# Optimization experiments

Hardware: AMD Instinct MI355X
Metric: run time of the kernel (lower is better)

## Reference

```python
import jax, jax.numpy as jnp
import numpy as np

B, N, D, F, L, R = 16, 1024, 256, 128, 2, 2


def setup_inputs() -> dict:
    key = jax.random.key(0)
    ks = jax.random.split(key, 12)
    s = 0.05
    return {
        "node_embed": jax.random.normal(ks[0], (B, N, D), jnp.float32),
        "input_x": jax.random.normal(ks[1], (B, F), jnp.float32),
        "adj": jax.random.randint(ks[2], (R, B, N, N), 0, 2, jnp.int32),
        "WQi_w": jax.random.normal(ks[3], (L, F, F), jnp.float32) * s,
        "WQi_b": jnp.zeros((L, F), jnp.float32),
        "WQ_w": jax.random.normal(ks[4], (L, D + F, D), jnp.float32) * s,
        "WQ_b": jnp.zeros((L, D), jnp.float32),
        "WK_w": jax.random.normal(ks[5], (L, R, D + F, D), jnp.float32) * s,
        "WK_b": jnp.zeros((L, R, D), jnp.float32),
        "WV_w": jax.random.normal(ks[6], (L, R, D + F, D), jnp.float32) * s,
        "WV_b": jnp.zeros((L, R, D), jnp.float32),
        "WF_w": jax.random.normal(ks[7], (L, R * D, D), jnp.float32) * s,
        "WF_b": jnp.zeros((L, D), jnp.float32),
        "ln_g": jnp.ones((L, D), jnp.float32),
        "ln_b": jnp.zeros((L, D), jnp.float32),
    }


def _layer_norm(x, g, b, eps=1e-5):
    mu = jnp.mean(x, axis=-1, keepdims=True)
    var = jnp.var(x, axis=-1, keepdims=True)
    return (x - mu) * jax.lax.rsqrt(var + eps) * g + b


def reference(node_embed, input_x, adj, WQi_w, WQi_b, WQ_w, WQ_b,
              WK_w, WK_b, WV_w, WV_b, WF_w, WF_b, ln_g, ln_b):
    scale = 1.0 / (D ** 0.5)
    h = node_embed
    for l in range(L):
        # input feature projection, broadcast over nodes
        x1 = input_x @ WQi_w[l] + WQi_b[l]              # (B, F)
        x1 = jnp.broadcast_to(x1[:, None, :], (h.shape[0], h.shape[1], F))
        qc = jnp.concatenate([h, x1], axis=-1)          # (B, N, D+F)
        q = qc @ WQ_w[l] + WQ_b[l]                      # (B, N, D)
        outs = []
        for r in range(R):
            k = qc @ WK_w[l, r] + WK_b[l, r]            # (B, N, D)
            v = qc @ WV_w[l, r] + WV_b[l, r]            # (B, N, D)
            scores = jnp.einsum('bnd,bmd->bnm', q, k) * scale
            scores = jnp.where(adj[r] == 0, -1e9, scores)
            alpha = jax.nn.softmax(scores, axis=-1)
            outs.append(jnp.einsum('bnm,bmd->bnd', alpha, v))
        h_concat = jnp.concatenate(outs, axis=-1)       # (B, N, R*D)
        h_fused = jax.nn.relu(h_concat @ WF_w[l] + WF_b[l])
        h = _layer_norm(h + h_fused, ln_g[l], ln_b[l])
    return h
```

## Files before the change

kernel.cpp:

```cpp
#include <hip/hip_runtime.h>
#include <hip/hip_bf16.h>

#define BB 16
#define NN 1024
#define DD 256
#define FF_ 128
#define LL 2
#define RR 2
#define DF 384
#define MM (BB*NN)
#define NPROJ 1280
#define PK 768
#define CSC 0.09016844f

typedef __attribute__((ext_vector_type(8))) short s16x8;
typedef __attribute__((ext_vector_type(4))) float f32x4;
typedef __attribute__((ext_vector_type(16))) float f32x16;
typedef __attribute__((ext_vector_type(2))) unsigned int u32x2;
typedef __attribute__((ext_vector_type(4))) unsigned int u32x4;
typedef __attribute__((ext_vector_type(4))) unsigned short us16x4;

__device__ __forceinline__ unsigned short f2bf(float f){
  unsigned u = __builtin_bit_cast(unsigned, f);
  u += 0x7fff + ((u >> 16) & 1);
  return (unsigned short)(u >> 16);
}

__device__ __forceinline__ void gload16(const void* g, void* l){
  __builtin_amdgcn_global_load_lds(
      (const __attribute__((address_space(1))) unsigned int*)g,
      (__attribute__((address_space(3))) unsigned int*)l, 16, 0, 0);
}

#define MFMA16(a,b,c) __builtin_amdgcn_mfma_f32_16x16x32_bf16((a),(b),(c),0,0,0)
#define MFMA32(a,b,c) __builtin_amdgcn_mfma_f32_32x32x16_bf16((a),(b),(c),0,0,0)

#define PREP_WT   3840
#define PREP_WTF  1024
#define PREP_BALL 10
#define PREP_X1   16
#define PREP_H    2048
#define PREP_TOT  (PREP_WT+PREP_WTF+PREP_BALL+PREP_X1+PREP_H)
#define PREP_ADJ  8192
#define PREP_ALL  (PREP_TOT+PREP_ADJ)

__global__ __launch_bounds__(256) void prep(
    const float* __restrict__ node, const float* __restrict__ inx,
    const float* __restrict__ WQi_w, const float* __restrict__ WQi_b,
    const float* __restrict__ WQ_w, const float* __restrict__ WK_w,
    const float* __restrict__ WV_w, const float* __restrict__ WQ_b,
    const float* __restrict__ WK_b, const float* __restrict__ WV_b,
    const float* __restrict__ WF_w, const int* __restrict__ adj,
    unsigned short* __restrict__ wtall, unsigned short* __restrict__ wtf,
    float* __restrict__ ball, unsigned short* __restrict__ x1bf,
    unsigned short* __restrict__ hbf, unsigned long long* __restrict__ bits){
  int bid = blockIdx.x, t = threadIdx.x;
  if (bid < PREP_WT){
    int o = bid*256 + t;
    int l = o / (NPROJ*DF); int oo = o - l*(NPROJ*DF);
    int n = oo / DF, k = oo - n*DF;
    const float* WQ = WQ_w + (size_t)l*DF*256;
    const float* WK = WK_w + (size_t)l*RR*DF*256;
    const float* WV = WV_w + (size_t)l*RR*DF*256;
    float v;
    if (n < 256)      v = WQ[(size_t)k*256 + n] * CSC;
    else if (n < 768) v = WK[(size_t)((n-256)>>8)*(DF*256) + (size_t)k*256 + ((n-256)&255)];
    else              v = WV[(size_t)((n-768)>>8)*(DF*256) + (size_t)k*256 + ((n-768)&255)];
    wtall[o] = f2bf(v);
  } else if (bid < PREP_WT + PREP_WTF){
    int o = (bid - PREP_WT)*256 + t;
    int l = o >> 17; int oo = o & 131071;
    int n = oo >> 9, k = oo & 511;
    wtf[o] = f2bf(WF_w[(size_t)l*512*256 + (size_t)k*256 + n]);
  } else if (bid < PREP_WT + PREP_WTF + PREP_BALL){
    int o = (bid - PREP_WT - PREP_WTF)*256 + t;
    if (o < 2*NPROJ){
      int l = o / NPROJ, n = o - l*NPROJ;
      float v = (n < 256) ? WQ_b[l*256 + n] * CSC
              : (n < 768) ? WK_b[(size_t)l*512 + (n-256)]
                          : WV_b[(size_t)l*512 + (n-768)];
      ball[o] = v;
    }
  } else if (bid < PREP_WT + PREP_WTF + PREP_BALL + PREP_X1){
    int o = (bid - PREP_WT - PREP_WTF - PREP_BALL)*256 + t;
    int l = o >> 11, bj = o & 2047;
    int b = bj >> 7, j = bj & 127;
    const float* w = WQi_w + (size_t)l*FF_*FF_;
    float s = WQi_b[l*FF_ + j];
    for (int i = 0; i < FF_; ++i) s += inx[b*FF_ + i] * w[i*FF_ + j];
    x1bf[o] = f2bf(s);
  } else if (bid < PREP_TOT){
    int o = (bid - (PREP_TOT - PREP_H))*256 + t;
    const float4* src = (const float4*)node + (size_t)o*2;
    float4 a = src[0], c = src[1];
    uint4 pk;
    pk.x = (unsigned)f2bf(a.x) | ((unsigned)f2bf(a.y) << 16);
    pk.y = (unsigned)f2bf(a.z) | ((unsigned)f2bf(a.w) << 16);
    pk.z = (unsigned)f2bf(c.x) | ((unsigned)f2bf(c.y) << 16);
    pk.w = (unsigned)f2bf(c.z) | ((unsigned)f2bf(c.w) << 16);
    *(uint4*)(hbf + (size_t)o*8) = pk;
  } else {
    int w = t >> 6, lane = t & 63;
    size_t row = (size_t)(bid - PREP_TOT) * 4 + w;
    const int* a = adj + row * NN;
    unsigned long long* brow = bits + row * 16;
    #pragma unroll
    for (int j = 0; j < 16; ++j){
      unsigned long long m = __ballot(a[j*64 + lane] != 0);
      if (lane == 0) brow[j] = m;
    }
  }
}

__global__ __launch_bounds__(256) void gemm_big(const unsigned short* __restrict__ hbf,
    const unsigned short* __restrict__ x1l, const unsigned short* __restrict__ Wt,
    const float* __restrict__ bias, unsigned short* __restrict__ POUT,
    unsigned short* __restrict__ vtall){
  __shared__ unsigned short As[2][128*32];
  __shared__ unsigned short Bs[2][128*32];
  int t = threadIdx.x, lane = t & 63, w = t >> 6;
  int wr = w >> 1, wc = w & 1, l15 = lane & 15, lhi = lane >> 4;
  int bm = blockIdx.x, bn = blockIdx.y, bb = bm >> 3;
  f32x4 acc[4][4];
  #pragma unroll
  for (int m = 0; m < 4; ++m)
    #pragma unroll
    for (int n = 0; n < 4; ++n) acc[m][n] = (f32x4){0.f,0.f,0.f,0.f};

  auto STAGE = [&](int bi, int kk){
    #pragma unroll
    for (int i = 0; i < 2; ++i){
      int base = w*2048 + i*1024;
      int off = base + lane*16;
      int row = off >> 6, cb = off & 63;
      const char* asrc = (kk < 8)
        ? (const char*)hbf + ((size_t)(bm*128 + row)*256 + kk*32)*2 + cb
        : (const char*)x1l + ((size_t)bb*128 + (kk-8)*32)*2 + cb;
      gload16(asrc, (char*)As[bi] + base);
      gload16((const char*)Wt + ((size_t)(bn*128 + row)*DF + kk*32)*2 + cb,
              (char*)Bs[bi] + base);
    }
  };

  STAGE(0, 0);
  for (int kk = 0; kk < 12; ++kk){
    int cur = kk & 1;
    if (kk + 1 < 12){
      STAGE(cur ^ 1, kk + 1);
      asm volatile("s_waitcnt vmcnt(4)" ::: "memory");
    } else {
      asm volatile("s_waitcnt vmcnt(0)" ::: "memory");
    }
    __builtin_amdgcn_s_barrier();
    __builtin_amdgcn_sched_barrier(0);
    s16x8 af[4], bfr[4];
    #pragma unroll
    for (int m = 0; m < 4; ++m) af[m]  = *(const s16x8*)&As[cur][(wr*64 + m*16 + l15)*32 + lhi*8];
    #pragma unroll
    for (int n = 0; n < 4; ++n) bfr[n] = *(const s16x8*)&Bs[cur][(wc*64 + n*16 + l15)*32 + lhi*8];
    __builtin_amdgcn_s_setprio(1);
    #pragma unroll
    for (int m = 0; m < 4; ++m)
      #pragma unroll
      for (int n = 0; n < 4; ++n)
        acc[m][n] = MFMA16(af[m], bfr[n], acc[m][n]);
    __builtin_amdgcn_s_setprio(0);
    __builtin_amdgcn_s_barrier();
  }

  if (bn < 6){
    #pragma unroll
    for (int n = 0; n < 4; ++n){
      int gn = bn*128 + wc*64 + n*16 + l15;
      float bv = bias[gn];
      #pragma unroll
      for (int m = 0; m < 4; ++m){
        int gm = bm*128 + wr*64 + m*16 + lhi*4;
        #pragma unroll
        for (int i = 0; i < 4; ++i)
          POUT[(size_t)(gm + i)*PK + gn] = f2bf(acc[m][n][i] + bv);
      }
    }
  } else {
    #pragma unroll
    for (int n = 0; n < 4; ++n){
      int gn = bn*128 + wc*64 + n*16 + l15;
      float bv = bias[gn];
      int rv = gn - 768;
      int r = rv >> 8, d = rv & 255;
      #pragma unroll
      for (int m = 0; m < 4; ++m){
        int mb = (bm & 7)*128 + wr*64 + m*16 + lhi*4;
        us16x4 pk;
        #pragma unroll
        for (int i = 0; i < 4; ++i) pk[i] = f2bf(acc[m][n][i] + bv);
        *(us16x4*)(vtall + ((size_t)((r*16 + bb)*256 + d))*NN + mb) = pk;
      }
    }
  }
}

__global__ __launch_bounds__(512, 1) void attn12(const unsigned short* __restrict__ P,
    const unsigned short* __restrict__ VT, const unsigned long long* __restrict__ bits,
    unsigned short* __restrict__ hc){
  __shared__ char smem[147456];

  int t = threadIdx.x, lane = t & 63, w = t >> 6;
  int h = lane >> 5, l31 = lane & 31;
  int qsub = w >> 1, dh = w & 1;
  int F = blockIdx.x;
  int xcd = F & 7, j = F >> 3;
  int qt = j & 7;
  int gidx = xcd*4 + (j >> 3);
  int b = gidx & 15, r = gidx >> 4;

  size_t kcol = 256 + (size_t)r*256;
  const unsigned short* Vb = VT + ((size_t)(r*16 + b))*256*NN;
  int qrow = qt*128 + qsub*32 + l31;

  s16x8 qf[16];
  {
    const unsigned short* qp = P + ((size_t)(b*NN + qrow))*PK + h*8;
    #pragma unroll
    for (int d_ = 0; d_ < 16; ++d_) qf[d_] = *(const s16x8*)(qp + d_*16);
  }

  {
    const unsigned long long* bb0 = bits + ((size_t)(r*BB + b)*NN + qt*128)*16;
    unsigned long long* ml = (unsigned long long*)(smem + 131072);
    #pragma unroll
    for (int i = 0; i < 4; ++i){
      int idx = t + i*512;
      int kt = idx >> 7, row = idx & 127;
      ml[kt*128 + row] = bb0[(size_t)row*16 + kt];
    }
  }

  f32x16 acc[4];
  #pragma unroll
  for (int dt = 0; dt < 4; ++dt)
    #pragma unroll
    for (int i = 0; i < 16; ++i) acc[dt][i] = 0.f;
  float mrow = -3e38f, lrow = 0.f;

  auto STAGE = [&](int buf, int kt){
    char* base = smem + buf*65536;
    #pragma unroll
    for (int i = 0; i < 4; ++i){
      int o = i*8192 + t*16;
      int kr = o >> 9, cb = o & 511;
      int lcb = cb ^ ((kr & 31) << 4);
      gload16((const char*)P + ((size_t)(b*NN + kt*64 + kr)*PK + kcol)*2 + lcb,
              base + o);
    }
    #pragma unroll
    for (int i = 0; i < 4; ++i){
      int o = i*8192 + t*16;
      int p = o >> 8, rem = o & 255;
      int lrem = rem ^ ((p & 15) << 4);
      int drow = p + (lrem >> 7)*128, col = lrem & 127;
      gload16((const char*)Vb + ((size_t)drow*NN + kt*64)*2 + col,
              base + 32768 + o);
    }
  };

  STAGE(0, 0);
  __syncthreads();

  for (int kt = 0; kt < 16; ++kt){
    int cur = kt & 1;
    if (kt + 1 < 16){
      STAGE(cur ^ 1, kt + 1);
      asm volatile("s_waitcnt vmcnt(8)" ::: "memory");
    } else {
      asm volatile("s_waitcnt vmcnt(0)" ::: "memory");
    }
    __builtin_amdgcn_s_barrier();
    __builtin_amdgcn_sched_barrier(0);

    unsigned long long mwv64 = *(const unsigned long long*)
        (smem + 131072 + kt*1024 + (qsub*32 + l31)*8);

    const char* Kc = smem + cur*65536;
    const char* Vc = smem + cur*65536 + 32768;

    f32x16 st0, st1;
    #pragma unroll
    for (int i = 0; i < 16; ++i){ st0[i] = 0.f; st1[i] = 0.f; }
    int swzk = l31 << 4;
    const char* kb0 = Kc + l31*512;
    const char* kb1 = Kc + (32 + l31)*512;
    #pragma unroll
    for (int d_ = 0; d_ < 16; ++d_){
      int co = (d_*32 + h*16) ^ swzk;
      s16x8 kf0 = *(const s16x8*)(kb0 + co);
      s16x8 kf1 = *(const s16x8*)(kb1 + co);
      st0 = MFMA32(kf0, qf[d_], st0);
      st1 = MFMA32(kf1, qf[d_], st1);
    }

    auto PROC = [&](f32x16 st, unsigned mw, int vcol){
      #pragma unroll
      for (int rr = 0; rr < 16; ++rr){
        int kb = (rr & 3) + 8*(rr >> 2) + 4*h;
        st[rr] = ((mw >> kb) & 1u) ? st[rr] : -1.443e9f;
      }
      float t8[8];
      #pragma unroll
      for (int p = 0; p < 8; ++p) t8[p] = fmaxf(st[p], st[p+8]);
      #pragma unroll
      for (int p = 0; p < 4; ++p) t8[p] = fmaxf(t8[p], t8[p+4]);
      float tm = fmaxf(fmaxf(t8[0], t8[1]), fmaxf(t8[2], t8[3]));
      tm = fmaxf(tm, __shfl_xor(tm, 32));
      if (tm > mrow + 10.f){
        float f = exp2f(mrow - tm);
        mrow = tm;
        lrow *= f;
        #pragma unroll
        for (int dt = 0; dt < 4; ++dt)
          #pragma unroll
          for (int i = 0; i < 16; ++i) acc[dt][i] *= f;
      }
      #pragma unroll
      for (int rr = 0; rr < 16; ++rr) st[rr] = exp2f(st[rr] - mrow);
      #pragma unroll
      for (int p = 0; p < 8; ++p) t8[p] = st[p] + st[p+8];
      #pragma unroll
      for (int p = 0; p < 4; ++p) t8[p] = t8[p] + t8[p+4];
      float rs = (t8[0] + t8[1]) + (t8[2] + t8[3]);
      rs += __shfl_xor(rs, 32);
      lrow += rs;

      unsigned pk[8];
      #pragma unroll
      for (int p = 0; p < 8; ++p){
        unsigned rpk;
        float lo = st[p*2], hi = st[p*2+1];
        asm("v_cvt_pk_bf16_f32 %0, %1, %2" : "=v"(rpk) : "v"(lo), "v"(hi));
        pk[p] = rpk;
      }
      unsigned sA = h ? pk[0] : pk[2], sB = h ? pk[1] : pk[3];
      unsigned sC = h ? pk[4] : pk[6], sD = h ? pk[5] : pk[7];
      unsigned rxA = (unsigned)__shfl_xor((int)sA, 32);
      unsigned rxB = (unsigned)__shfl_xor((int)sB, 32);
      unsigned rxC = (unsigned)__shfl_xor((int)sC, 32);
      unsigned rxD = (unsigned)__shfl_xor((int)sD, 32);
      u32x4 pv0, pv1;
      pv0[0] = h ? rxA : pk[0]; pv0[1] = h ? rxB : pk[1];
      pv0[2] = h ? pk[2] : rxA; pv0[3] = h ? pk[3] : rxB;
      pv1[0] = h ? rxC : pk[4]; pv1[1] = h ? rxD : pk[5];
      pv1[2] = h ? pk[6] : rxC; pv1[3] = h ? pk[7] : rxD;
      s16x8 pa0 = __builtin_bit_cast(s16x8, pv0);
      s16x8 pa1 = __builtin_bit_cast(s16x8, pv1);

      #pragma unroll
      for (int dt = 0; dt < 4; ++dt){
        int p = dt*32 + l31;
        int swzv = (p & 15) << 4;
        const char* vbase = Vc + p*256;
        s16x8 vf0 = *(const s16x8*)(vbase + ((dh*128 + vcol + h*16) ^ swzv));
        acc[dt] = MFMA32(vf0, pa0, acc[dt]);
        s16x8 vf1 = *(const s16x8*)(vbase + ((dh*128 + vcol + 32 + h*16) ^ swzv));
        acc[dt] = MFMA32(vf1, pa1, acc[dt]);
      }
    };
    PROC(st0, (unsigned)mwv64, 0);
    PROC(st1, (unsigned)(mwv64 >> 32), 64);

    __builtin_amdgcn_s_barrier();
  }

  float inv = 1.f / lrow;
  unsigned short* hrow = hc + ((size_t)(b*NN + qrow))*(RR*DD) + r*DD;
  #pragma unroll
  for (int dt = 0; dt < 4; ++dt){
    #pragma unroll
    for (int g = 0; g < 4; ++g){
      float a0 = acc[dt][g*4+0]*inv, a1 = acc[dt][g*4+1]*inv;
      float a2 = acc[dt][g*4+2]*inv, a3 = acc[dt][g*4+3]*inv;
      unsigned r0, r1;
      asm("v_cvt_pk_bf16_f32 %0, %1, %2" : "=v"(r0) : "v"(a0), "v"(a1));
      asm("v_cvt_pk_bf16_f32 %0, %1, %2" : "=v"(r1) : "v"(a2), "v"(a3));
      int d = dh*128 + dt*32 + 8*g + 4*h;
      u32x2 pv; pv[0] = r0; pv[1] = r1;
      *(u32x2*)(hrow + d) = pv;
    }
  }
}

__global__ __launch_bounds__(256) void gemm_ff(const unsigned short* __restrict__ A,
    const unsigned short* __restrict__ Wt, const float* __restrict__ bias,
    float* __restrict__ out){
  __shared__ unsigned short As[2][128*32];
  __shared__ unsigned short Bs[2][128*32];
  int t = threadIdx.x, lane = t & 63, w = t >> 6;
  int wr = w >> 1, wc = w & 1, l15 = lane & 15, lhi = lane >> 4;
  int bm = blockIdx.x, bn = blockIdx.y;
  f32x4 acc[4][4];
  #pragma unroll
  for (int m = 0; m < 4; ++m)
    #pragma unroll
    for (int n = 0; n < 4; ++n) acc[m][n] = (f32x4){0.f,0.f,0.f,0.f};

  auto STAGE = [&](int bi, int kk){
    #pragma unroll
    for (int i = 0; i < 2; ++i){
      int base = w*2048 + i*1024;
      int off = base + lane*16;
      int row = off >> 6, cb = off & 63;
      gload16((const char*)A  + ((size_t)(bm*128 + row)*512 + kk*32)*2 + cb,
              (char*)As[bi] + base);
      gload16((const char*)Wt + ((size_t)(bn*128 + row)*512 + kk*32)*2 + cb,
              (char*)Bs[bi] + base);
    }
  };

  STAGE(0, 0);
  for (int kk = 0; kk < 16; ++kk){
    int cur = kk & 1;
    if (kk + 1 < 16){
      STAGE(cur ^ 1, kk + 1);
      asm volatile("s_waitcnt vmcnt(4)" ::: "memory");
    } else {
      asm volatile("s_waitcnt vmcnt(0)" ::: "memory");
    }
    __builtin_amdgcn_s_barrier();
    __builtin_amdgcn_sched_barrier(0);
    s16x8 af[4], bfr[4];
    #pragma unroll
    for (int m = 0; m < 4; ++m) af[m]  = *(const s16x8*)&As[cur][(wr*64 + m*16 + l15)*32 + lhi*8];
    #pragma unroll
    for (int n = 0; n < 4; ++n) bfr[n] = *(const s16x8*)&Bs[cur][(wc*64 + n*16 + l15)*32 + lhi*8];
    __builtin_amdgcn_s_setprio(1);
    #pragma unroll
    for (int m = 0; m < 4; ++m)
      #pragma unroll
      for (int n = 0; n < 4; ++n)
        acc[m][n] = MFMA16(af[m], bfr[n], acc[m][n]);
    __builtin_amdgcn_s_setprio(0);
    __builtin_amdgcn_s_barrier();
  }

  #pragma unroll
  for (int n = 0; n < 4; ++n){
    int gn = bn*128 + wc*64 + n*16 + l15;
    float bv = bias[gn];
    #pragma unroll
    for (int m = 0; m < 4; ++m){
      int gm = bm*128 + wr*64 + m*16 + lhi*4;
      #pragma unroll
      for (int i = 0; i < 4; ++i)
        out[(size_t)(gm + i)*DD + gn] = acc[m][n][i] + bv;
    }
  }
}

template<int WRITEH>
__global__ __launch_bounds__(256) void ln_res2(const float* __restrict__ ff,
    const float* __restrict__ hin, const float* __restrict__ g,
    const float* __restrict__ bv, float* __restrict__ hout,
    unsigned short* __restrict__ hbf){
  int w = threadIdx.x >> 6, lane = threadIdx.x & 63;
  size_t row = (size_t)blockIdx.x * 4 + w;
  f32x4 fv = *(const f32x4*)(ff  + row*DD + lane*4);
  f32x4 hv = *(const f32x4*)(hin + row*DD + lane*4);
  float x[4], s = 0.f, ss = 0.f;
  #pragma unroll
  for (int j = 0; j < 4; ++j){ x[j] = fmaxf(fv[j], 0.f) + hv[j]; s += x[j]; ss += x[j]*x[j]; }
  #pragma unroll
  for (int xm = 1; xm < 64; xm <<= 1){ s += __shfl_xor(s, xm); ss += __shfl_xor(ss, xm); }
  float mu = s * (1.f/256.f);
  float var = ss * (1.f/256.f) - mu*mu;
  float rstd = rsqrtf(var + 1e-5f);
  f32x4 o;
  #pragma unroll
  for (int j = 0; j < 4; ++j){ int c = lane*4 + j; o[j] = (x[j]-mu)*rstd*g[c] + bv[c]; }
  *(f32x4*)(hout + row*DD + lane*4) = o;
  if (WRITEH){
    uint2 pv;
    pv.x = (unsigned)f2bf(o[0]) | ((unsigned)f2bf(o[1]) << 16);
    pv.y = (unsigned)f2bf(o[2]) | ((unsigned)f2bf(o[3]) << 16);
    *(uint2*)(hbf + row*DD + lane*4) = pv;
  }
}

extern "C" void kernel_launch(void* const* d_in, const int* in_sizes, int n_in,
                              void* d_out, int out_size, void* d_ws, size_t ws_size,
                              hipStream_t stream){
  (void)in_sizes; (void)n_in; (void)out_size; (void)ws_size;
  const float* node  = (const float*)d_in[0];
  const float* inx   = (const float*)d_in[1];
  const int*   adj   = (const int*)d_in[2];
  const float* WQi_w = (const float*)d_in[3];
  const float* WQi_b = (const float*)d_in[4];
  const float* WQ_w  = (const float*)d_in[5];
  const float* WQ_b  = (const float*)d_in[6];
  const float* WK_w  = (const float*)d_in[7];
  const float* WK_b  = (const float*)d_in[8];
  const float* WV_w  = (const float*)d_in[9];
  const float* WV_b  = (const float*)d_in[10];
  const float* WF_w  = (const float*)d_in[11];
  const float* WF_b  = (const float*)d_in[12];
  const float* ln_g  = (const float*)d_in[13];
  const float* ln_b  = (const float*)d_in[14];
  float* hout = (float*)d_out;

  char* wsp = (char*)d_ws;
  auto alloc = [&](size_t n){ char* p = wsp; wsp += (n + 255) & ~(size_t)255; return p; };
  unsigned long long* bits = (unsigned long long*)alloc((size_t)RR*BB*NN*16*8);
  unsigned short* wtall = (unsigned short*)alloc((size_t)2*NPROJ*DF*2);
  unsigned short* wtf   = (unsigned short*)alloc((size_t)2*DD*512*2);
  float*          ball  = (float*)alloc((size_t)2*NPROJ*4);
  unsigned short* x1bf  = (unsigned short*)alloc((size_t)2*BB*FF_*2);
  unsigned short* hbf   = (unsigned short*)alloc((size_t)MM*DD*2);
  unsigned short* POUT  = (unsigned short*)alloc((size_t)MM*PK*2);
  unsigned short* vtall = (unsigned short*)alloc((size_t)RR*BB*DD*NN*2);
  unsigned short* hc    = (unsigned short*)alloc((size_t)MM*512*2);
  float*          ffo   = (float*)alloc((size_t)MM*DD*4);

  prep<<<PREP_ALL, 256, 0, stream>>>(node, inx, WQi_w, WQi_b, WQ_w, WK_w, WV_w,
                                     WQ_b, WK_b, WV_b, WF_w, adj,
                                     wtall, wtf, ball, x1bf, hbf, bits);

  for (int l = 0; l < LL; ++l){
    gemm_big<<<dim3(128,10), 256, 0, stream>>>(hbf, x1bf + (size_t)l*BB*FF_,
        wtall + (size_t)l*NPROJ*DF, ball + (size_t)l*NPROJ, POUT, vtall);

    attn12<<<256, 512, 0, stream>>>(POUT, vtall, bits, hc);

    gemm_ff<<<dim3(128,2), 256, 0, stream>>>(hc, wtf + (size_t)l*DD*512, WF_b + l*DD, ffo);

    if (l == 0) ln_res2<1><<<MM/4, 256, 0, stream>>>(ffo, node, ln_g, ln_b, hout, hbf);
    else        ln_res2<0><<<MM/4, 256, 0, stream>>>(ffo, (const float*)hout,
                                                     ln_g + DD, ln_b + DD, hout, nullptr);
  }
}
```

Before: 297.1 us.

## Software-pipeline attention: overlap QK of tile k with PV of tile k-1, triple buffer

The attention kernel now uses 32-key tiles instead of 64, held in three LDS buffers so loads run two tiles ahead. Each iteration computes the QK^T scores of the current tile and then the PV MFMAs of the previous tile, keeping the probability fragments in registers across iterations. This lets MFMA work overlap with the softmax arithmetic and shortens the serial dependency inside each iteration. The trade-offs are twice as many iterations and barriers, a smaller LDS footprint, and extra live registers for the carried fragments.

```diff
diff --git a/kernel.cpp b/kernel.cpp
--- a/kernel.cpp
+++ b/kernel.cpp
@@ -200,10 +200,10 @@
   }
 }
 
-__global__ __launch_bounds__(512, 1) void attn12(const unsigned short* __restrict__ P,
+__global__ __launch_bounds__(512, 1) void attn13(const unsigned short* __restrict__ P,
     const unsigned short* __restrict__ VT, const unsigned long long* __restrict__ bits,
     unsigned short* __restrict__ hc){
-  __shared__ char smem[147456];
+  __shared__ char smem[114688];
 
   int t = threadIdx.x, lane = t & 63, w = t >> 6;
   int h = lane >> 5, l31 = lane & 31;
@@ -226,13 +226,13 @@
   }
 
   {
-    const unsigned long long* bb0 = bits + ((size_t)(r*BB + b)*NN + qt*128)*16;
-    unsigned long long* ml = (unsigned long long*)(smem + 131072);
-    #pragma unroll
-    for (int i = 0; i < 4; ++i){
+    const unsigned* src32 = (const unsigned*)(bits + ((size_t)(r*BB + b)*NN + qt*128)*16);
+    unsigned* ml = (unsigned*)(smem + 98304);
+    #pragma unroll
+    for (int i = 0; i < 8; ++i){
       int idx = t + i*512;
       int kt = idx >> 7, row = idx & 127;
-      ml[kt*128 + row] = bb0[(size_t)row*16 + kt];
+      ml[kt*128 + row] = src32[row*32 + kt];
     }
   }
 
@@ -242,132 +242,140 @@
     #pragma unroll
     for (int i = 0; i < 16; ++i) acc[dt][i] = 0.f;
   float mrow = -3e38f, lrow = 0.f;
-
-  auto STAGE = [&](int buf, int kt){
-    char* base = smem + buf*65536;
-    #pragma unroll
-    for (int i = 0; i < 4; ++i){
+  s16x8 pa0{}, pa1{};
+
+  auto STAGE = [&](char* base, int kt){
+    #pragma unroll
+    for (int i = 0; i < 2; ++i){
       int o = i*8192 + t*16;
       int kr = o >> 9, cb = o & 511;
-      int lcb = cb ^ ((kr & 31) << 4);
-      gload16((const char*)P + ((size_t)(b*NN + kt*64 + kr)*PK + kcol)*2 + lcb,
+      int lcb = cb ^ (kr << 4);
+      gload16((const char*)P + ((size_t)(b*NN + kt*32 + kr)*PK + kcol)*2 + lcb,
               base + o);
     }
     #pragma unroll
-    for (int i = 0; i < 4; ++i){
+    for (int i = 0; i < 2; ++i){
       int o = i*8192 + t*16;
       int p = o >> 8, rem = o & 255;
       int lrem = rem ^ ((p & 15) << 4);
-      int drow = p + (lrem >> 7)*128, col = lrem & 127;
-      gload16((const char*)Vb + ((size_t)drow*NN + kt*64)*2 + col,
-              base + 32768 + o);
+      int quarter = lrem >> 6, col = lrem & 63;
+      gload16((const char*)Vb + ((size_t)(p + quarter*64)*NN + kt*32)*2 + col,
+              base + 16384 + o);
     }
   };
 
-  STAGE(0, 0);
+  char* bufA = smem;
+  char* bufB = smem + 32768;
+  char* bufC = smem + 65536;
+  STAGE(bufA, 0);
+  STAGE(bufB, 1);
   __syncthreads();
-
-  for (int kt = 0; kt < 16; ++kt){
-    int cur = kt & 1;
-    if (kt + 1 < 16){
-      STAGE(cur ^ 1, kt + 1);
-      asm volatile("s_waitcnt vmcnt(8)" ::: "memory");
-    } else {
-      asm volatile("s_waitcnt vmcnt(0)" ::: "memory");
-    }
+  char* prv = bufC;
+  char* cur = bufA;
+  char* nxt = bufB;
+
+  for (int kt = 0; kt < 32; ++kt){
+    if (kt == 31) asm volatile("s_waitcnt vmcnt(0)" ::: "memory");
+    else          asm volatile("s_waitcnt vmcnt(4)" ::: "memory");
     __builtin_amdgcn_s_barrier();
     __builtin_amdgcn_sched_barrier(0);
 
-    unsigned long long mwv64 = *(const unsigned long long*)
-        (smem + 131072 + kt*1024 + (qsub*32 + l31)*8);
-
-    const char* Kc = smem + cur*65536;
-    const char* Vc = smem + cur*65536 + 32768;
-
-    f32x16 st0, st1;
-    #pragma unroll
-    for (int i = 0; i < 16; ++i){ st0[i] = 0.f; st1[i] = 0.f; }
+    unsigned mw0 = *(const unsigned*)(smem + 98304 + (kt*128 + qsub*32 + l31)*4);
+
+    f32x16 st;
+    #pragma unroll
+    for (int i = 0; i < 16; ++i) st[i] = 0.f;
+    const char* kbase = cur + l31*512;
     int swzk = l31 << 4;
-    const char* kb0 = Kc + l31*512;
-    const char* kb1 = Kc + (32 + l31)*512;
     #pragma unroll
     for (int d_ = 0; d_ < 16; ++d_){
-      int co = (d_*32 + h*16) ^ swzk;
-      s16x8 kf0 = *(const s16x8*)(kb0 + co);
-      s16x8 kf1 = *(const s16x8*)(kb1 + co);
-      st0 = MFMA32(kf0, qf[d_], st0);
-      st1 = MFMA32(kf1, qf[d_], st1);
-    }
-
-    auto PROC = [&](f32x16 st, unsigned mw, int vcol){
-      #pragma unroll
-      for (int rr = 0; rr < 16; ++rr){
-        int kb = (rr & 3) + 8*(rr >> 2) + 4*h;
-        st[rr] = ((mw >> kb) & 1u) ? st[rr] : -1.443e9f;
-      }
-      float t8[8];
-      #pragma unroll
-      for (int p = 0; p < 8; ++p) t8[p] = fmaxf(st[p], st[p+8]);
-      #pragma unroll
-      for (int p = 0; p < 4; ++p) t8[p] = fmaxf(t8[p], t8[p+4]);
-      float tm = fmaxf(fmaxf(t8[0], t8[1]), fmaxf(t8[2], t8[3]));
-      tm = fmaxf(tm, __shfl_xor(tm, 32));
-      if (tm > mrow + 10.f){
-        float f = exp2f(mrow - tm);
-        mrow = tm;
-        lrow *= f;
-        #pragma unroll
-        for (int dt = 0; dt < 4; ++dt)
-          #pragma unroll
-          for (int i = 0; i < 16; ++i) acc[dt][i] *= f;
-      }
-      #pragma unroll
-      for (int rr = 0; rr < 16; ++rr) st[rr] = exp2f(st[rr] - mrow);
-      #pragma unroll
-      for (int p = 0; p < 8; ++p) t8[p] = st[p] + st[p+8];
-      #pragma unroll
-      for (int p = 0; p < 4; ++p) t8[p] = t8[p] + t8[p+4];
-      float rs = (t8[0] + t8[1]) + (t8[2] + t8[3]);
-      rs += __shfl_xor(rs, 32);
-      lrow += rs;
-
-      unsigned pk[8];
-      #pragma unroll
-      for (int p = 0; p < 8; ++p){
-        unsigned rpk;
-        float lo = st[p*2], hi = st[p*2+1];
-        asm("v_cvt_pk_bf16_f32 %0, %1, %2" : "=v"(rpk) : "v"(lo), "v"(hi));
-        pk[p] = rpk;
-      }
-      unsigned sA = h ? pk[0] : pk[2], sB = h ? pk[1] : pk[3];
-      unsigned sC = h ? pk[4] : pk[6], sD = h ? pk[5] : pk[7];
-      unsigned rxA = (unsigned)__shfl_xor((int)sA, 32);
-      unsigned rxB = (unsigned)__shfl_xor((int)sB, 32);
-      unsigned rxC = (unsigned)__shfl_xor((int)sC, 32);
-      unsigned rxD = (unsigned)__shfl_xor((int)sD, 32);
-      u32x4 pv0, pv1;
-      pv0[0] = h ? rxA : pk[0]; pv0[1] = h ? rxB : pk[1];
-      pv0[2] = h ? pk[2] : rxA; pv0[3] = h ? pk[3] : rxB;
-      pv1[0] = h ? rxC : pk[4]; pv1[1] = h ? rxD : pk[5];
-      pv1[2] = h ? pk[6] : rxC; pv1[3] = h ? pk[7] : rxD;
-      s16x8 pa0 = __builtin_bit_cast(s16x8, pv0);
-      s16x8 pa1 = __builtin_bit_cast(s16x8, pv1);
-
+      s16x8 kf = *(const s16x8*)(kbase + ((d_*32 + h*16) ^ swzk));
+      st = MFMA32(kf, qf[d_], st);
+    }
+
+    if (kt > 0){
       #pragma unroll
       for (int dt = 0; dt < 4; ++dt){
-        int p = dt*32 + l31;
-        int swzv = (p & 15) << 4;
-        const char* vbase = Vc + p*256;
-        s16x8 vf0 = *(const s16x8*)(vbase + ((dh*128 + vcol + h*16) ^ swzv));
+        int vr = dh*128 + dt*32 + l31;
+        int qn = vr & 63, quarter = vr >> 6;
+        int swzv = (qn & 15) << 4;
+        const char* vbase = prv + 16384 + qn*256;
+        s16x8 vf0 = *(const s16x8*)(vbase + ((quarter*64 + h*16) ^ swzv));
         acc[dt] = MFMA32(vf0, pa0, acc[dt]);
-        s16x8 vf1 = *(const s16x8*)(vbase + ((dh*128 + vcol + 32 + h*16) ^ swzv));
+        s16x8 vf1 = *(const s16x8*)(vbase + ((quarter*64 + 32 + h*16) ^ swzv));
         acc[dt] = MFMA32(vf1, pa1, acc[dt]);
       }
-    };
-    PROC(st0, (unsigned)mwv64, 0);
-    PROC(st1, (unsigned)(mwv64 >> 32), 64);
+    }
+
+    unsigned mw = mw0 >> (h*4);
+    #pragma unroll
+    for (int rr = 0; rr < 16; ++rr){
+      const int kb = (rr & 3) + 8*(rr >> 2);
+      st[rr] = ((mw >> kb) & 1u) ? st[rr] : -1.443e9f;
+    }
+    float t8[8];
+    #pragma unroll
+    for (int p = 0; p < 8; ++p) t8[p] = fmaxf(st[p], st[p+8]);
+    #pragma unroll
+    for (int p = 0; p < 4; ++p) t8[p] = fmaxf(t8[p], t8[p+4]);
+    float tm = fmaxf(fmaxf(t8[0], t8[1]), fmaxf(t8[2], t8[3]));
+    tm = fmaxf(tm, __shfl_xor(tm, 32));
+    if (tm > mrow + 10.f){
+      float f = exp2f(mrow - tm);
+      mrow = tm;
+      lrow *= f;
+      #pragma unroll
+      for (int dt = 0; dt < 4; ++dt)
+        #pragma unroll
+        for (int i = 0; i < 16; ++i) acc[dt][i] *= f;
+    }
+    #pragma unroll
+    for (int rr = 0; rr < 16; ++rr) st[rr] = exp2f(st[rr] - mrow);
+    #pragma unroll
+    for (int p = 0; p < 8; ++p) t8[p] = st[p] + st[p+8];
+    #pragma unroll
+    for (int p = 0; p < 4; ++p) t8[p] = t8[p] + t8[p+4];
+    float rs = (t8[0] + t8[1]) + (t8[2] + t8[3]);
+    rs += __shfl_xor(rs, 32);
+    lrow += rs;
+
+    unsigned pk[8];
+    #pragma unroll
+    for (int p = 0; p < 8; ++p){
+      unsigned rpk;
+      float lo = st[p*2], hi = st[p*2+1];
+      asm("v_cvt_pk_bf16_f32 %0, %1, %2" : "=v"(rpk) : "v"(lo), "v"(hi));
+      pk[p] = rpk;
+    }
+    unsigned sA = h ? pk[0] : pk[2], sB = h ? pk[1] : pk[3];
+    unsigned sC = h ? pk[4] : pk[6], sD = h ? pk[5] : pk[7];
+    unsigned rxA = (unsigned)__shfl_xor((int)sA, 32);
+    unsigned rxB = (unsigned)__shfl_xor((int)sB, 32);
+    unsigned rxC = (unsigned)__shfl_xor((int)sC, 32);
+    unsigned rxD = (unsigned)__shfl_xor((int)sD, 32);
+    u32x4 pv0, pv1;
+    pv0[0] = h ? rxA : pk[0]; pv0[1] = h ? rxB : pk[1];
+    pv0[2] = h ? pk[2] : rxA; pv0[3] = h ? pk[3] : rxB;
+    pv1[0] = h ? rxC : pk[4]; pv1[1] = h ? rxD : pk[5];
+    pv1[2] = h ? pk[6] : rxC; pv1[3] = h ? pk[7] : rxD;
+    pa0 = __builtin_bit_cast(s16x8, pv0);
+    pa1 = __builtin_bit_cast(s16x8, pv1);
 
     __builtin_amdgcn_s_barrier();
+    if (kt + 2 < 32) STAGE(prv, kt + 2);
+    char* tmp = prv; prv = cur; cur = nxt; nxt = tmp;
+  }
+
+  #pragma unroll
+  for (int dt = 0; dt < 4; ++dt){
+    int vr = dh*128 + dt*32 + l31;
+    int qn = vr & 63, quarter = vr >> 6;
+    int swzv = (qn & 15) << 4;
+    const char* vbase = prv + 16384 + qn*256;
+    s16x8 vf0 = *(const s16x8*)(vbase + ((quarter*64 + h*16) ^ swzv));
+    acc[dt] = MFMA32(vf0, pa0, acc[dt]);
+    s16x8 vf1 = *(const s16x8*)(vbase + ((quarter*64 + 32 + h*16) ^ swzv));
+    acc[dt] = MFMA32(vf1, pa1, acc[dt]);
   }
 
   float inv = 1.f / lrow;
@@ -526,7 +534,7 @@
     gemm_big<<<dim3(128,10), 256, 0, stream>>>(hbf, x1bf + (size_t)l*BB*FF_,
         wtall + (size_t)l*NPROJ*DF, ball + (size_t)l*NPROJ, POUT, vtall);
 
-    attn12<<<256, 512, 0, stream>>>(POUT, vtall, bits, hc);
+    attn13<<<256, 512, 0, stream>>>(POUT, vtall, bits, hc);
 
     gemm_ff<<<dim3(128,2), 256, 0, stream>>>(hc, wtf + (size_t)l*DD*512, WF_b + l*DD, ffo);
 
```

Measured after the change: 301.1 us. Within noise of the previous version (+1.4%).

## Shrink attention blocks to 64 query rows and 32-key tiles for two blocks/CU

Applied to the files above, without the earlier changes.

The attention kernel moves from 512-thread blocks with 128 query rows and 64-key tiles to 256-thread blocks with 64 query rows and 32-key tiles. Shared memory per block is halved so two blocks can co-reside per CU, and the grid doubles to 512 blocks for better load balance across CUs. The mask layout, K/V staging swizzles and V fragment addressing are rewritten to match the smaller tiles. In exchange there are twice as many loop iterations and barriers, and each block must load K/V from memory on its own.

```diff
diff --git a/kernel.cpp b/kernel.cpp
--- a/kernel.cpp
+++ b/kernel.cpp
@@ -200,23 +200,23 @@
   }
 }
 
-__global__ __launch_bounds__(512, 1) void attn12(const unsigned short* __restrict__ P,
+__global__ __launch_bounds__(256, 2) void attn14(const unsigned short* __restrict__ P,
     const unsigned short* __restrict__ VT, const unsigned long long* __restrict__ bits,
     unsigned short* __restrict__ hc){
-  __shared__ char smem[147456];
+  __shared__ char smem[73728];
 
   int t = threadIdx.x, lane = t & 63, w = t >> 6;
   int h = lane >> 5, l31 = lane & 31;
   int qsub = w >> 1, dh = w & 1;
   int F = blockIdx.x;
   int xcd = F & 7, j = F >> 3;
-  int qt = j & 7;
-  int gidx = xcd*4 + (j >> 3);
+  int qt = j & 15;
+  int gidx = xcd*4 + (j >> 4);
   int b = gidx & 15, r = gidx >> 4;
 
   size_t kcol = 256 + (size_t)r*256;
   const unsigned short* Vb = VT + ((size_t)(r*16 + b))*256*NN;
-  int qrow = qt*128 + qsub*32 + l31;
+  int qrow = qt*64 + qsub*32 + l31;
 
   s16x8 qf[16];
   {
@@ -226,13 +226,13 @@
   }
 
   {
-    const unsigned long long* bb0 = bits + ((size_t)(r*BB + b)*NN + qt*128)*16;
-    unsigned long long* ml = (unsigned long long*)(smem + 131072);
-    #pragma unroll
-    for (int i = 0; i < 4; ++i){
-      int idx = t + i*512;
-      int kt = idx >> 7, row = idx & 127;
-      ml[kt*128 + row] = bb0[(size_t)row*16 + kt];
+    const unsigned* src32 = (const unsigned*)(bits + ((size_t)(r*BB + b)*NN + qt*64)*16);
+    unsigned* ml = (unsigned*)(smem + 65536);
+    #pragma unroll
+    for (int i = 0; i < 8; ++i){
+      int idx = t + i*256;
+      int kt = idx >> 6, row = idx & 63;
+      ml[kt*64 + row] = src32[row*32 + kt];
     }
   }
 
@@ -244,32 +244,32 @@
   float mrow = -3e38f, lrow = 0.f;
 
   auto STAGE = [&](int buf, int kt){
-    char* base = smem + buf*65536;
+    char* base = smem + buf*32768;
     #pragma unroll
     for (int i = 0; i < 4; ++i){
-      int o = i*8192 + t*16;
+      int o = i*4096 + t*16;
       int kr = o >> 9, cb = o & 511;
-      int lcb = cb ^ ((kr & 31) << 4);
-      gload16((const char*)P + ((size_t)(b*NN + kt*64 + kr)*PK + kcol)*2 + lcb,
+      int lcb = cb ^ (kr << 4);
+      gload16((const char*)P + ((size_t)(b*NN + kt*32 + kr)*PK + kcol)*2 + lcb,
               base + o);
     }
     #pragma unroll
     for (int i = 0; i < 4; ++i){
-      int o = i*8192 + t*16;
+      int o = i*4096 + t*16;
       int p = o >> 8, rem = o & 255;
       int lrem = rem ^ ((p & 15) << 4);
-      int drow = p + (lrem >> 7)*128, col = lrem & 127;
-      gload16((const char*)Vb + ((size_t)drow*NN + kt*64)*2 + col,
-              base + 32768 + o);
+      int quarter = lrem >> 6, col = lrem & 63;
+      gload16((const char*)Vb + ((size_t)(p + quarter*64)*NN + kt*32)*2 + col,
+              base + 16384 + o);
     }
   };
 
   STAGE(0, 0);
   __syncthreads();
 
-  for (int kt = 0; kt < 16; ++kt){
+  for (int kt = 0; kt < 32; ++kt){
     int cur = kt & 1;
-    if (kt + 1 < 16){
+    if (kt + 1 < 32){
       STAGE(cur ^ 1, kt + 1);
       asm volatile("s_waitcnt vmcnt(8)" ::: "memory");
     } else {
@@ -278,94 +278,87 @@
     __builtin_amdgcn_s_barrier();
     __builtin_amdgcn_sched_barrier(0);
 
-    unsigned long long mwv64 = *(const unsigned long long*)
-        (smem + 131072 + kt*1024 + (qsub*32 + l31)*8);
-
-    const char* Kc = smem + cur*65536;
-    const char* Vc = smem + cur*65536 + 32768;
-
-    f32x16 st0, st1;
-    #pragma unroll
-    for (int i = 0; i < 16; ++i){ st0[i] = 0.f; st1[i] = 0.f; }
+    unsigned mw0 = *(const unsigned*)(smem + 65536 + (kt*64 + qsub*32 + l31)*4);
+
+    const char* Kc = smem + cur*32768;
+    const char* Vc = smem + cur*32768 + 16384;
+
+    f32x16 st;
+    #pragma unroll
+    for (int i = 0; i < 16; ++i) st[i] = 0.f;
+    const char* kbase = Kc + l31*512;
     int swzk = l31 << 4;
-    const char* kb0 = Kc + l31*512;
-    const char* kb1 = Kc + (32 + l31)*512;
     #pragma unroll
     for (int d_ = 0; d_ < 16; ++d_){
-      int co = (d_*32 + h*16) ^ swzk;
-      s16x8 kf0 = *(const s16x8*)(kb0 + co);
-      s16x8 kf1 = *(const s16x8*)(kb1 + co);
-      st0 = MFMA32(kf0, qf[d_], st0);
-      st1 = MFMA32(kf1, qf[d_], st1);
-    }
-
-    auto PROC = [&](f32x16 st, unsigned mw, int vcol){
+      s16x8 kf = *(const s16x8*)(kbase + ((d_*32 + h*16) ^ swzk));
+      st = MFMA32(kf, qf[d_], st);
+    }
+
+    unsigned mw = mw0 >> (h*4);
+    #pragma unroll
+    for (int rr = 0; rr < 16; ++rr){
+      const int kb = (rr & 3) + 8*(rr >> 2);
+      st[rr] = ((mw >> kb) & 1u) ? st[rr] : -1.443e9f;
+    }
+    float t8[8];
+    #pragma unroll
+    for (int p = 0; p < 8; ++p) t8[p] = fmaxf(st[p], st[p+8]);
+    #pragma unroll
+    for (int p = 0; p < 4; ++p) t8[p] = fmaxf(t8[p], t8[p+4]);
+    float tm = fmaxf(fmaxf(t8[0], t8[1]), fmaxf(t8[2], t8[3]));
+    tm = fmaxf(tm, __shfl_xor(tm, 32));
+    if (tm > mrow + 10.f){
+      float f = exp2f(mrow - tm);
+      mrow = tm;
+      lrow *= f;
       #pragma unroll
-      for (int rr = 0; rr < 16; ++rr){
-        int kb = (rr & 3) + 8*(rr >> 2) + 4*h;
-        st[rr] = ((mw >> kb) & 1u) ? st[rr] : -1.443e9f;
-      }
-      float t8[8];
-      #pragma unroll
-      for (int p = 0; p < 8; ++p) t8[p] = fmaxf(st[p], st[p+8]);
-      #pragma unroll
-      for (int p = 0; p < 4; ++p) t8[p] = fmaxf(t8[p], t8[p+4]);
-      float tm = fmaxf(fmaxf(t8[0], t8[1]), fmaxf(t8[2], t8[3]));
-      tm = fmaxf(tm, __shfl_xor(tm, 32));
-      if (tm > mrow + 10.f){
-        float f = exp2f(mrow - tm);
-        mrow = tm;
-        lrow *= f;
+      for (int dt = 0; dt < 4; ++dt)
         #pragma unroll
-        for (int dt = 0; dt < 4; ++dt)
-          #pragma unroll
-          for (int i = 0; i < 16; ++i) acc[dt][i] *= f;
-      }
-      #pragma unroll
-      for (int rr = 0; rr < 16; ++rr) st[rr] = exp2f(st[rr] - mrow);
-      #pragma unroll
-      for (int p = 0; p < 8; ++p) t8[p] = st[p] + st[p+8];
-      #pragma unroll
-      for (int p = 0; p < 4; ++p) t8[p] = t8[p] + t8[p+4];
-      float rs = (t8[0] + t8[1]) + (t8[2] + t8[3]);
-      rs += __shfl_xor(rs, 32);
-      lrow += rs;
-
-      unsigned pk[8];
-      #pragma unroll
-      for (int p = 0; p < 8; ++p){
-        unsigned rpk;
-        float lo = st[p*2], hi = st[p*2+1];
-        asm("v_cvt_pk_bf16_f32 %0, %1, %2" : "=v"(rpk) : "v"(lo), "v"(hi));
-        pk[p] = rpk;
-      }
-      unsigned sA = h ? pk[0] : pk[2], sB = h ? pk[1] : pk[3];
-      unsigned sC = h ? pk[4] : pk[6], sD = h ? pk[5] : pk[7];
-      unsigned rxA = (unsigned)__shfl_xor((int)sA, 32);
-      unsigned rxB = (unsigned)__shfl_xor((int)sB, 32);
-      unsigned rxC = (unsigned)__shfl_xor((int)sC, 32);
-      unsigned rxD = (unsigned)__shfl_xor((int)sD, 32);
-      u32x4 pv0, pv1;
-      pv0[0] = h ? rxA : pk[0]; pv0[1] = h ? rxB : pk[1];
-      pv0[2] = h ? pk[2] : rxA; pv0[3] = h ? pk[3] : rxB;
-      pv1[0] = h ? rxC : pk[4]; pv1[1] = h ? rxD : pk[5];
-      pv1[2] = h ? pk[6] : rxC; pv1[3] = h ? pk[7] : rxD;
-      s16x8 pa0 = __builtin_bit_cast(s16x8, pv0);
-      s16x8 pa1 = __builtin_bit_cast(s16x8, pv1);
-
-      #pragma unroll
-      for (int dt = 0; dt < 4; ++dt){
-        int p = dt*32 + l31;
-        int swzv = (p & 15) << 4;
-        const char* vbase = Vc + p*256;
-        s16x8 vf0 = *(const s16x8*)(vbase + ((dh*128 + vcol + h*16) ^ swzv));
-        acc[dt] = MFMA32(vf0, pa0, acc[dt]);
-        s16x8 vf1 = *(const s16x8*)(vbase + ((dh*128 + vcol + 32 + h*16) ^ swzv));
-        acc[dt] = MFMA32(vf1, pa1, acc[dt]);
-      }
-    };
-    PROC(st0, (unsigned)mwv64, 0);
-    PROC(st1, (unsigned)(mwv64 >> 32), 64);
+        for (int i = 0; i < 16; ++i) acc[dt][i] *= f;
+    }
+    #pragma unroll
+    for (int rr = 0; rr < 16; ++rr) st[rr] = exp2f(st[rr] - mrow);
+    #pragma unroll
+    for (int p = 0; p < 8; ++p) t8[p] = st[p] + st[p+8];
+    #pragma unroll
+    for (int p = 0; p < 4; ++p) t8[p] = t8[p] + t8[p+4];
+    float rs = (t8[0] + t8[1]) + (t8[2] + t8[3]);
+    rs += __shfl_xor(rs, 32);
+    lrow += rs;
+
+    unsigned pk[8];
+    #pragma unroll
+    for (int p = 0; p < 8; ++p){
+      unsigned rpk;
+      float lo = st[p*2], hi = st[p*2+1];
+      asm("v_cvt_pk_bf16_f32 %0, %1, %2" : "=v"(rpk) : "v"(lo), "v"(hi));
+      pk[p] = rpk;
+    }
+    unsigned sA = h ? pk[0] : pk[2], sB = h ? pk[1] : pk[3];
+    unsigned sC = h ? pk[4] : pk[6], sD = h ? pk[5] : pk[7];
+    unsigned rxA = (unsigned)__shfl_xor((int)sA, 32);
+    unsigned rxB = (unsigned)__shfl_xor((int)sB, 32);
+    unsigned rxC = (unsigned)__shfl_xor((int)sC, 32);
+    unsigned rxD = (unsigned)__shfl_xor((int)sD, 32);
+    u32x4 pv0, pv1;
+    pv0[0] = h ? rxA : pk[0]; pv0[1] = h ? rxB : pk[1];
+    pv0[2] = h ? pk[2] : rxA; pv0[3] = h ? pk[3] : rxB;
+    pv1[0] = h ? rxC : pk[4]; pv1[1] = h ? rxD : pk[5];
+    pv1[2] = h ? pk[6] : rxC; pv1[3] = h ? pk[7] : rxD;
+    s16x8 pa0 = __builtin_bit_cast(s16x8, pv0);
+    s16x8 pa1 = __builtin_bit_cast(s16x8, pv1);
+
+    #pragma unroll
+    for (int dt = 0; dt < 4; ++dt){
+      int vr = dh*128 + dt*32 + l31;
+      int p = vr & 63, quarter = vr >> 6;
+      int swzv = (p & 15) << 4;
+      const char* vbase = Vc + p*256;
+      s16x8 vf0 = *(const s16x8*)(vbase + ((quarter*64 + h*16) ^ swzv));
+      acc[dt] = MFMA32(vf0, pa0, acc[dt]);
+      s16x8 vf1 = *(const s16x8*)(vbase + ((quarter*64 + 32 + h*16) ^ swzv));
+      acc[dt] = MFMA32(vf1, pa1, acc[dt]);
+    }
 
     __builtin_amdgcn_s_barrier();
   }
@@ -526,7 +519,7 @@
     gemm_big<<<dim3(128,10), 256, 0, stream>>>(hbf, x1bf + (size_t)l*BB*FF_,
         wtall + (size_t)l*NPROJ*DF, ball + (size_t)l*NPROJ, POUT, vtall);
 
-    attn12<<<256, 512, 0, stream>>>(POUT, vtall, bits, hc);
+    attn14<<<512, 256, 0, stream>>>(POUT, vtall, bits, hc);
 
     gemm_ff<<<dim3(128,2), 256, 0, stream>>>(hc, wtf + (size_t)l*DD*512, WF_b + l*DD, ffo);
 
```

After: 302.1 us. About the same (+1.7%).
